# Performance work log

Hardware: AMD Instinct MI355X
Metric: run time of the kernel (lower is better)

Reference implementation:

```python
import jax, jax.numpy as jnp
import numpy as np

K = 5          # involution kernel size
GC = 8         # group_channels
EPS = 1e-5     # BatchNorm eps


def _unfold(x, k):
    """torch nn.Unfold(k, dilation=1, padding=(k-1)//2, stride=1) equivalent.
    x: [B,C,H,W] -> [B, C, k*k, H, W] with channel-major ordering matching
    torch's view(b, groups, group_channels, k*k, h, w)."""
    p = (k - 1) // 2
    B, C, H, W = x.shape
    xp = jnp.pad(x, ((0, 0), (0, 0), (p, p), (p, p)))
    # fixed small loop over k*k taps (k=5 -> 25 slices)
    taps = [xp[:, :, i:i + H, j:j + W] for i in range(k) for j in range(k)]
    return jnp.stack(taps, axis=2)  # [B, C, k*k, H, W]


def involution_fwd(x, w1, b1, bn_gamma, bn_beta, bn_mean, bn_var, w2, b2):
    B, C, H, W = x.shape
    groups = C // GC
    # conv1: 1x1 conv + BN(eval) + ReLU6
    y = jnp.einsum('bchw,oc->bohw', x, w1) + b1[None, :, None, None]
    scale = bn_gamma / jnp.sqrt(bn_var + EPS)
    y = y * scale[None, :, None, None] + (bn_beta - bn_mean * scale)[None, :, None, None]
    y = jnp.clip(y, 0.0, 6.0)
    # conv2: 1x1 conv -> per-pixel kernels [B, k*k*groups, H, W]
    kern = jnp.einsum('bchw,oc->bohw', y, w2) + b2[None, :, None, None]
    kern = kern.reshape(B, groups, 1, K * K, H, W)  # broadcast over group_channels
    # unfold + weighted sum over k*k taps
    patches = _unfold(x, K).reshape(B, groups, GC, K * K, H, W)
    out = (kern * patches).sum(axis=3).reshape(B, C, H, W)
    return out


def setup_inputs() -> dict:
    key = jax.random.key(0)
    ks = jax.random.split(key, 9)
    B, C, H, W = 8, 256, 64, 64
    cr = C // 4                       # reduction_ratio = 4
    groups = C // GC                  # 32
    return {
        'x': jax.random.normal(ks[0], (B, C, H, W), jnp.float32),
        'w1': jax.random.normal(ks[1], (cr, C), jnp.float32) * 0.05,
        'b1': jax.random.normal(ks[2], (cr,), jnp.float32) * 0.05,
        'bn_gamma': jax.random.uniform(ks[3], (cr,), jnp.float32, 0.5, 1.5),
        'bn_beta': jax.random.normal(ks[4], (cr,), jnp.float32) * 0.05,
        'bn_mean': jax.random.normal(ks[5], (cr,), jnp.float32) * 0.05,
        'bn_var': jax.random.uniform(ks[6], (cr,), jnp.float32, 0.5, 1.5),
        'w2': jax.random.normal(ks[7], (K * K * groups, cr), jnp.float32) * 0.05,
        'b2': jax.random.normal(ks[8], (K * K * groups,), jnp.float32) * 0.05,
    }


def reference(x, w1, b1, bn_gamma, bn_beta, bn_mean, bn_var, w2, b2):
    return involution_fwd(x, w1, b1, bn_gamma, bn_beta, bn_mean, bn_var, w2, b2)
```

## Files before the change

kernel.cpp:

```cpp
#include <hip/hip_runtime.h>

#define BB   8
#define CC   256
#define HH   64
#define WW   64
#define CR   64
#define NG   32
#define GC   8
#define KK   25
#define HW   (HH*WW)

typedef __attribute__((ext_vector_type(8))) short short8;
typedef __attribute__((ext_vector_type(4))) float f32x4;

__device__ __forceinline__ unsigned short f2bf(float f) {
    unsigned u = __builtin_bit_cast(unsigned, f);
    u += 0x7FFFu + ((u >> 16) & 1u);
    return (unsigned short)(u >> 16);
}

__global__ __launch_bounds__(256) void prep_kernel(
    const float* __restrict__ w1, const float* __restrict__ b1,
    const float* __restrict__ gamma, const float* __restrict__ beta,
    const float* __restrict__ mean, const float* __restrict__ var,
    const float* __restrict__ w2,
    unsigned short* __restrict__ w1a, float* __restrict__ b1f,
    unsigned short* __restrict__ w2p)
{
    int gid = blockIdx.x;
    if (gid < 256) {
        int idx = gid * 256 + threadIdx.x;
        int j  = idx & 7;
        int l  = (idx >> 3) & 63;
        int ki = (idx >> 9) & 1;
        int nt = (idx >> 10) & 1;
        int g  = idx >> 11;
        int nl = nt * 16 + (l & 15);
        int k  = ki * 32 + (l >> 4) * 8 + j;
        float v = (nl < KK) ? w2[(g * KK + nl) * CR + k] : 0.0f;
        w2p[idx] = f2bf(v);
    } else {
        int idx = (gid - 256) * 256 + threadIdx.x;
        int j  = idx & 7;
        int l  = (idx >> 3) & 63;
        int mt = (idx >> 9) & 3;
        int ki = (idx >> 11) & 7;
        int r  = mt * 16 + (l & 15);
        int c  = ki * 32 + (l >> 4) * 8 + j;
        float scale = gamma[r] * rsqrtf(var[r] + 1e-5f);
        w1a[idx] = f2bf(w1[r * CC + c] * scale);
        if (idx < CR) {
            float s = gamma[idx] * rsqrtf(var[idx] + 1e-5f);
            b1f[idx] = (b1[idx] - mean[idx]) * s + beta[idx];
        }
    }
}

__global__ __launch_bounds__(256) void conv1_kernel(
    const float* __restrict__ x, const unsigned short* __restrict__ w1a,
    const float* __restrict__ b1f, unsigned short* __restrict__ ybf)
{
    const int tid  = threadIdx.x;
    const int h    = blockIdx.x;
    const int b    = blockIdx.y;
    const int lane = tid & 63;
    const int wv   = tid >> 6;
    const int l15  = lane & 15;
    const int q    = lane >> 4;
    const int px   = wv * 16 + l15;

    const float*  xc   = x + (size_t)b * CC * HW + h * WW + px;
    const short8* w1a8 = (const short8*)w1a;

    f32x4 cfr[4];
    #pragma unroll
    for (int mt = 0; mt < 4; ++mt) cfr[mt] = (f32x4){0.f, 0.f, 0.f, 0.f};

    #pragma unroll
    for (int ki = 0; ki < 8; ++ki) {
        short8 bfr;
        #pragma unroll
        for (int j = 0; j < 8; ++j) {
            float v = xc[(ki * 32 + q * 8 + j) * HW];
            bfr[j] = (short)f2bf(v);
        }
        #pragma unroll
        for (int mt = 0; mt < 4; ++mt) {
            short8 afr = w1a8[(ki * 4 + mt) * 64 + lane];
            cfr[mt] = __builtin_amdgcn_mfma_f32_16x16x32_bf16(afr, bfr, cfr[mt], 0, 0, 0);
        }
    }

    unsigned short* yb = ybf + ((size_t)(b * HH + h) * WW + px) * CR;
    #pragma unroll
    for (int mt = 0; mt < 4; ++mt) {
        unsigned pk[2];
        #pragma unroll
        for (int rp = 0; rp < 2; ++rp) {
            float v0 = cfr[mt][rp * 2 + 0] + b1f[mt * 16 + q * 4 + rp * 2 + 0];
            float v1 = cfr[mt][rp * 2 + 1] + b1f[mt * 16 + q * 4 + rp * 2 + 1];
            v0 = fminf(fmaxf(v0, 0.0f), 6.0f);
            v1 = fminf(fmaxf(v1, 0.0f), 6.0f);
            pk[rp] = (unsigned)f2bf(v0) | ((unsigned)f2bf(v1) << 16);
        }
        *(uint2*)(yb + mt * 16 + q * 4) = make_uint2(pk[0], pk[1]);
    }
}

__global__ __launch_bounds__(256, 2) void invol_kernel(
    const float* __restrict__ x, const unsigned short* __restrict__ ybf,
    const unsigned short* __restrict__ w2p, const float* __restrict__ b2,
    float* __restrict__ out)
{
    __shared__ float klds[4][32 * 68];

    const int tid  = threadIdx.x;
    const int bx   = blockIdx.x;
    const int hq   = bx >> 3;
    const int gs   = bx & 7;
    const int b    = blockIdx.y;
    const int lane = tid & 63;
    const int wv   = __builtin_amdgcn_readfirstlane(tid >> 6);
    const int g    = gs * 4 + wv;
    const int h0   = hq * 4;
    const int wq   = lane >> 3;
    const int ch   = lane & 7;
    const int w0   = wq * 8;
    const int l15  = lane & 15;
    const int q    = lane >> 4;
    float* kw = klds[wv];

    const short8* w2p8 = (const short8*)w2p;
    short8 bf[2][2];
    #pragma unroll
    for (int nt = 0; nt < 2; ++nt)
        #pragma unroll
        for (int ki = 0; ki < 2; ++ki)
            bf[nt][ki] = w2p8[((g * 2 + nt) * 2 + ki) * 64 + lane];
    float b2v[2];
    #pragma unroll
    for (int nt = 0; nt < 2; ++nt) {
        int t = nt * 16 + l15;
        b2v[nt] = b2[g * KK + min(t, KK - 1)];
    }

    float xw[8][12];
    const float* xch = x + (size_t)(b * CC + g * GC + ch) * HW;
    const bool wlo = (wq == 0), whi = (wq == 7);

    #define LOADROW(ridx_)                                                     \
    {                                                                          \
        int hh = h0 - 2 + (ridx_);                                             \
        int hc = min(max(hh, 0), HH - 1);                                      \
        const float* xr = xch + hc * WW;                                       \
        float2 elo = *(const float2*)(xr + max(w0 - 2, 0));                    \
        float4 m0  = *(const float4*)(xr + w0);                                \
        float4 m1  = *(const float4*)(xr + w0 + 4);                            \
        float2 ehi = *(const float2*)(xr + min(w0 + 8, WW - 2));               \
        xw[ridx_][0]  = wlo ? 0.0f : elo.x;                                    \
        xw[ridx_][1]  = wlo ? 0.0f : elo.y;                                    \
        xw[ridx_][2]  = m0.x; xw[ridx_][3] = m0.y;                             \
        xw[ridx_][4]  = m0.z; xw[ridx_][5] = m0.w;                             \
        xw[ridx_][6]  = m1.x; xw[ridx_][7] = m1.y;                             \
        xw[ridx_][8]  = m1.z; xw[ridx_][9] = m1.w;                             \
        xw[ridx_][10] = whi ? 0.0f : ehi.x;                                    \
        xw[ridx_][11] = whi ? 0.0f : ehi.y;                                    \
    }

    LOADROW(0) LOADROW(1) LOADROW(2) LOADROW(3) LOADROW(4)

    #pragma unroll
    for (int ho = 0; ho < 4; ++ho) {
        const int h = h0 + ho;

        const unsigned short* yb = ybf + (size_t)(b * HH + h) * WW * CR;
        f32x4 cfr[4][2];
        #pragma unroll
        for (int mt = 0; mt < 4; ++mt)
            #pragma unroll
            for (int nt = 0; nt < 2; ++nt)
                cfr[mt][nt] = (f32x4){b2v[nt], b2v[nt], b2v[nt], b2v[nt]};
        #pragma unroll
        for (int ki = 0; ki < 2; ++ki)
            #pragma unroll
            for (int mt = 0; mt < 4; ++mt) {
                short8 afr = *(const short8*)(yb + (mt * 16 + l15) * CR + ki * 32 + q * 8);
                #pragma unroll
                for (int nt = 0; nt < 2; ++nt)
                    cfr[mt][nt] = __builtin_amdgcn_mfma_f32_16x16x32_bf16(
                        afr, bf[nt][ki], cfr[mt][nt], 0, 0, 0);
            }
        #pragma unroll
        for (int mt = 0; mt < 4; ++mt)
            #pragma unroll
            for (int nt = 0; nt < 2; ++nt)
                *(float4*)(&kw[(nt * 16 + l15) * 68 + mt * 16 + q * 4]) =
                    (float4){cfr[mt][nt][0], cfr[mt][nt][1], cfr[mt][nt][2], cfr[mt][nt][3]};

        float oacc[8];
        #pragma unroll
        for (int i = 0; i < 8; ++i) oacc[i] = 0.0f;

        #pragma unroll
        for (int di = 0; di < 5; ++di) {
            int hh = h + di - 2;
            if (hh >= 0 && hh < HH) {
                #pragma unroll
                for (int dj = 0; dj < 5; ++dj) {
                    float4 k0 = *(const float4*)(&kw[(di * 5 + dj) * 68 + w0]);
                    float4 k1 = *(const float4*)(&kw[(di * 5 + dj) * 68 + w0 + 4]);
                    #pragma unroll
                    for (int wi = 0; wi < 4; ++wi) {
                        oacc[wi]     = fmaf(k0[wi], xw[ho + di][wi + dj],     oacc[wi]);
                        oacc[wi + 4] = fmaf(k1[wi], xw[ho + di][wi + 4 + dj], oacc[wi + 4]);
                    }
                }
            }
        }

        float* op = out + ((size_t)(b * CC + g * GC + ch) * HH + h) * WW + w0;
        *(float4*)op       = (float4){oacc[0], oacc[1], oacc[2], oacc[3]};
        *(float4*)(op + 4) = (float4){oacc[4], oacc[5], oacc[6], oacc[7]};

        if (ho == 0) LOADROW(5)
        if (ho == 1) LOADROW(6)
        if (ho == 2) LOADROW(7)
    }
    #undef LOADROW
}

extern "C" void kernel_launch(void* const* d_in, const int* in_sizes, int n_in,
                              void* d_out, int out_size, void* d_ws, size_t ws_size,
                              hipStream_t stream) {
    const float* x     = (const float*)d_in[0];
    const float* w1    = (const float*)d_in[1];
    const float* b1    = (const float*)d_in[2];
    const float* gamma = (const float*)d_in[3];
    const float* beta  = (const float*)d_in[4];
    const float* mean  = (const float*)d_in[5];
    const float* var   = (const float*)d_in[6];
    const float* w2    = (const float*)d_in[7];
    const float* b2    = (const float*)d_in[8];
    float* out = (float*)d_out;

    char* ws = (char*)d_ws;
    unsigned short* w1a = (unsigned short*)ws;
    float*          b1f = (float*)(ws + 32768);
    unsigned short* w2p = (unsigned short*)(ws + 33024);
    unsigned short* ybf = (unsigned short*)(ws + 164096);

    prep_kernel<<<320, 256, 0, stream>>>(w1, b1, gamma, beta, mean, var, w2,
                                         w1a, b1f, w2p);
    conv1_kernel<<<dim3(HH, BB), 256, 0, stream>>>(x, w1a, b1f, ybf);
    invol_kernel<<<dim3(128, BB), 256, 0, stream>>>(x, ybf, w2p, b2, out);
}
```

Measured before the change: 132.9 us.

## Software-pipeline per-row kernel generation with double-buffered LDS and prefetched y rows

Restructures the per-row loop so the bf16 y fragments for row h+1 and the next x row are loaded before the involution FMA work on row h. The MFMA for the next row then writes into the other half of a double-buffered LDS region. This is meant to hide global-load latency behind compute. In exchange it doubles LDS use per block and holds more registers for the prefetched fragments, which may reduce occupancy.

```diff
diff --git a/kernel.cpp b/kernel.cpp
--- a/kernel.cpp
+++ b/kernel.cpp
@@ -112,7 +112,7 @@
     const unsigned short* __restrict__ w2p, const float* __restrict__ b2,
     float* __restrict__ out)
 {
-    __shared__ float klds[4][32 * 68];
+    __shared__ float klds[4][2][32 * 68];
 
     const int tid  = threadIdx.x;
     const int bx   = blockIdx.x;
@@ -128,7 +128,6 @@
     const int w0   = wq * 8;
     const int l15  = lane & 15;
     const int q    = lane >> 4;
-    float* kw = klds[wv];
 
     const short8* w2p8 = (const short8*)w2p;
     short8 bf[2][2];
@@ -142,6 +141,45 @@
     for (int nt = 0; nt < 2; ++nt) {
         int t = nt * 16 + l15;
         b2v[nt] = b2[g * KK + min(t, KK - 1)];
+    }
+
+    const unsigned short* ybase = ybf + (size_t)(b * HH) * WW * CR;
+
+    #define LOAD_AFR(dst_, h_)                                                 \
+    {                                                                          \
+        const unsigned short* yb_ = ybase + (size_t)(h_) * WW * CR;            \
+        _Pragma("unroll")                                                      \
+        for (int ki = 0; ki < 2; ++ki)                                         \
+            _Pragma("unroll")                                                  \
+            for (int mt = 0; mt < 4; ++mt)                                     \
+                (dst_)[ki * 4 + mt] = *(const short8*)(                        \
+                    yb_ + (mt * 16 + l15) * CR + ki * 32 + q * 8);             \
+    }
+
+    #define MFMA_STORE(src_, buf_)                                             \
+    {                                                                          \
+        float* kd_ = &klds[wv][buf_][0];                                       \
+        f32x4 cfr[4][2];                                                       \
+        _Pragma("unroll")                                                      \
+        for (int mt = 0; mt < 4; ++mt)                                         \
+            _Pragma("unroll")                                                  \
+            for (int nt = 0; nt < 2; ++nt)                                     \
+                cfr[mt][nt] = (f32x4){b2v[nt], b2v[nt], b2v[nt], b2v[nt]};     \
+        _Pragma("unroll")                                                      \
+        for (int ki = 0; ki < 2; ++ki)                                         \
+            _Pragma("unroll")                                                  \
+            for (int mt = 0; mt < 4; ++mt)                                     \
+                _Pragma("unroll")                                              \
+                for (int nt = 0; nt < 2; ++nt)                                 \
+                    cfr[mt][nt] = __builtin_amdgcn_mfma_f32_16x16x32_bf16(     \
+                        (src_)[ki * 4 + mt], bf[nt][ki], cfr[mt][nt], 0, 0, 0);\
+        _Pragma("unroll")                                                      \
+        for (int mt = 0; mt < 4; ++mt)                                         \
+            _Pragma("unroll")                                                  \
+            for (int nt = 0; nt < 2; ++nt)                                     \
+                *(float4*)(&kd_[(nt * 16 + l15) * 68 + mt * 16 + q * 4]) =     \
+                    (float4){cfr[mt][nt][0], cfr[mt][nt][1],                   \
+                             cfr[mt][nt][2], cfr[mt][nt][3]};                  \
     }
 
     float xw[8][12];
@@ -169,34 +207,21 @@
 
     LOADROW(0) LOADROW(1) LOADROW(2) LOADROW(3) LOADROW(4)
 
+    short8 afr[2][8];
+    LOAD_AFR(afr[0], h0)
+    MFMA_STORE(afr[0], 0)
+
     #pragma unroll
     for (int ho = 0; ho < 4; ++ho) {
-        const int h = h0 + ho;
-
-        const unsigned short* yb = ybf + (size_t)(b * HH + h) * WW * CR;
-        f32x4 cfr[4][2];
-        #pragma unroll
-        for (int mt = 0; mt < 4; ++mt)
-            #pragma unroll
-            for (int nt = 0; nt < 2; ++nt)
-                cfr[mt][nt] = (f32x4){b2v[nt], b2v[nt], b2v[nt], b2v[nt]};
-        #pragma unroll
-        for (int ki = 0; ki < 2; ++ki)
-            #pragma unroll
-            for (int mt = 0; mt < 4; ++mt) {
-                short8 afr = *(const short8*)(yb + (mt * 16 + l15) * CR + ki * 32 + q * 8);
-                #pragma unroll
-                for (int nt = 0; nt < 2; ++nt)
-                    cfr[mt][nt] = __builtin_amdgcn_mfma_f32_16x16x32_bf16(
-                        afr, bf[nt][ki], cfr[mt][nt], 0, 0, 0);
-            }
-        #pragma unroll
-        for (int mt = 0; mt < 4; ++mt)
-            #pragma unroll
-            for (int nt = 0; nt < 2; ++nt)
-                *(float4*)(&kw[(nt * 16 + l15) * 68 + mt * 16 + q * 4]) =
-                    (float4){cfr[mt][nt][0], cfr[mt][nt][1], cfr[mt][nt][2], cfr[mt][nt][3]};
-
+        const int h  = h0 + ho;
+        const int cb = ho & 1;
+
+        if (ho < 3) LOAD_AFR(afr[(ho + 1) & 1], h + 1)
+        if (ho == 0) LOADROW(5)
+        if (ho == 1) LOADROW(6)
+        if (ho == 2) LOADROW(7)
+
+        const float* kw = &klds[wv][cb][0];
         float oacc[8];
         #pragma unroll
         for (int i = 0; i < 8; ++i) oacc[i] = 0.0f;
@@ -222,11 +247,11 @@
         *(float4*)op       = (float4){oacc[0], oacc[1], oacc[2], oacc[3]};
         *(float4*)(op + 4) = (float4){oacc[4], oacc[5], oacc[6], oacc[7]};
 
-        if (ho == 0) LOADROW(5)
-        if (ho == 1) LOADROW(6)
-        if (ho == 2) LOADROW(7)
+        if (ho < 3) MFMA_STORE(afr[(ho + 1) & 1], (ho + 1) & 1)
     }
     #undef LOADROW
+    #undef LOAD_AFR
+    #undef MFMA_STORE
 }
 
 extern "C" void kernel_launch(void* const* d_in, const int* in_sizes, int n_in,
```

Measured after the change: 133.0 us. Within noise of the previous version (+0.1%).
